# Optimization experiments

Measured on AMD Instinct MI355X. Metric: run time of the kernel, lower is better.

## Reference

```python
import jax, jax.numpy as jnp
import numpy as np

EPS = 1e-5


def gated_graph_conv(x, edge_index, W, w_ih, w_hh, b_ih, b_hh):
    # W: [num_layers, C, C]; PyG pads input features up to out_channels C.
    N = x.shape[0]
    C = W.shape[1]
    if x.shape[1] < C:
        x = jnp.pad(x, ((0, 0), (0, C - x.shape[1])))
    src, dst = edge_index[0], edge_index[1]
    for i in range(W.shape[0]):
        m = x @ W[i]                                   # [N, C]
        agg = jax.ops.segment_sum(m[src], dst, num_segments=N)  # scatter-add aggr
        # GRUCell(agg, x)
        gi = agg @ w_ih.T + b_ih                       # [N, 3C]
        gh = x @ w_hh.T + b_hh
        ir, iz, in_ = jnp.split(gi, 3, axis=-1)
        hr, hz, hn = jnp.split(gh, 3, axis=-1)
        r = jax.nn.sigmoid(ir + hr)
        z = jax.nn.sigmoid(iz + hz)
        n = jnp.tanh(in_ + r * hn)
        x = (1.0 - z) * n + z * x
    return x


def batch_norm_eval(x, gamma, beta, mean, var):
    return (x - mean) * jax.lax.rsqrt(var + EPS) * gamma + beta


def _ggc_params(key, C):
    ks = jax.random.split(key, 5)
    s = 1.0 / np.sqrt(C)
    return (jax.random.uniform(ks[0], (4, C, C), minval=-s, maxval=s),
            jax.random.uniform(ks[1], (3 * C, C), minval=-s, maxval=s),
            jax.random.uniform(ks[2], (3 * C, C), minval=-s, maxval=s),
            jax.random.uniform(ks[3], (3 * C,), minval=-s, maxval=s),
            jax.random.uniform(ks[4], (3 * C,), minval=-s, maxval=s))


def _bn_params(key, C):
    ks = jax.random.split(key, 4)
    return (jax.random.normal(ks[0], (C,)) * 0.1 + 1.0,
            jax.random.normal(ks[1], (C,)) * 0.1,
            jax.random.normal(ks[2], (C,)) * 0.1,
            jax.random.uniform(ks[3], (C,), minval=0.5, maxval=1.5))


def setup_inputs() -> dict:
    key = jax.random.key(0)
    N, E, NF, NG, NA = 50000, 800000, 32, 256, 10
    ks = jax.random.split(key, 12)
    x = jax.random.normal(ks[0], (N, NF), dtype=jnp.float32)
    edge_index = jax.random.randint(ks[1], (2, E), 0, N, dtype=jnp.int64)
    batch = jnp.sort(jax.random.randint(ks[2], (N,), 0, NG, dtype=jnp.int64))
    c1 = _ggc_params(ks[3], NF)
    c2 = _ggc_params(ks[4], 64)
    c3 = _ggc_params(ks[5], 128)
    bn1 = _bn_params(ks[6], NF)
    bn2 = _bn_params(ks[7], 64)
    s1 = 1.0 / np.sqrt(128)
    fc1_W = jax.random.uniform(ks[8], (256, 128), minval=-s1, maxval=s1)
    fc1_b = jax.random.uniform(ks[9], (256,), minval=-s1, maxval=s1)
    s2 = 1.0 / np.sqrt(256)
    fc2_W = jax.random.uniform(ks[10], (NA, 256), minval=-s2, maxval=s2)
    fc2_b = jax.random.uniform(ks[11], (NA,), minval=-s2, maxval=s2)
    d = {"x": x, "edge_index": edge_index, "batch": batch,
         "fc1_W": fc1_W, "fc1_b": fc1_b, "fc2_W": fc2_W, "fc2_b": fc2_b}
    for name, p in (("conv1", c1), ("conv2", c2), ("conv3", c3)):
        d[name + "_W"], d[name + "_wih"], d[name + "_whh"], d[name + "_bih"], d[name + "_bhh"] = p
    for name, p in (("bn1", bn1), ("bn2", bn2)):
        d[name + "_gamma"], d[name + "_beta"], d[name + "_mean"], d[name + "_var"] = p
    return d


def reference(x, edge_index, batch,
              conv1_W, conv1_wih, conv1_whh, conv1_bih, conv1_bhh,
              conv2_W, conv2_wih, conv2_whh, conv2_bih, conv2_bhh,
              conv3_W, conv3_wih, conv3_whh, conv3_bih, conv3_bhh,
              bn1_gamma, bn1_beta, bn1_mean, bn1_var,
              bn2_gamma, bn2_beta, bn2_mean, bn2_var,
              fc1_W, fc1_b, fc2_W, fc2_b):
    NUM_GRAPHS = 256
    h = jax.nn.elu(gated_graph_conv(x, edge_index, conv1_W, conv1_wih, conv1_whh, conv1_bih, conv1_bhh))
    h = batch_norm_eval(h, bn1_gamma, bn1_beta, bn1_mean, bn1_var)
    h = jax.nn.elu(gated_graph_conv(h, edge_index, conv2_W, conv2_wih, conv2_whh, conv2_bih, conv2_bhh))
    h = batch_norm_eval(h, bn2_gamma, bn2_beta, bn2_mean, bn2_var)
    h = jax.nn.elu(gated_graph_conv(h, edge_index, conv3_W, conv3_wih, conv3_whh, conv3_bih, conv3_bhh))
    g = jax.ops.segment_sum(h, batch, num_segments=NUM_GRAPHS)  # global_add_pool
    g = jax.nn.elu(g @ fc1_W.T + fc1_b)
    # dropout is identity in eval mode
    return jax.nn.log_softmax(g @ fc2_W.T + fc2_b, axis=-1)
```

## Files before the change

### kernel.cpp

```cpp
#include <hip/hip_runtime.h>
#include <math.h>


#define EPS_BN 1e-5f

typedef short short8 __attribute__((ext_vector_type(8)));
typedef unsigned short u16x8 __attribute__((ext_vector_type(8)));
typedef float f32x4 __attribute__((ext_vector_type(4)));

__device__ __forceinline__ float elu_f(float v) {
    return v > 0.f ? v : expm1f(v);
}
__device__ __forceinline__ float sigmoid_f(float v) {
    return 1.f / (1.f + __expf(-v));
}
__device__ __forceinline__ float tanh_f(float v) {
    float e = __expf(2.f * v);
    return 1.f - 2.f / (e + 1.f);
}
__device__ __forceinline__ unsigned short f2bf(float f) {
    unsigned u = __float_as_uint(f);
    unsigned r = (u + 0x7FFF + ((u >> 16) & 1)) >> 16;
    return (unsigned short)r;
}
__device__ __forceinline__ float bf2f(unsigned short b) {
    return __uint_as_float(((unsigned)b) << 16);
}


__global__ __launch_bounds__(256) void hist_kernel(
    const int* __restrict__ ei, int* __restrict__ deg, int E, int N) {
    int part = blockIdx.x & 7;
    int blk = blockIdx.x >> 3;
    int nblk = gridDim.x >> 3;
    int lo = (int)((long)N * part >> 3);
    int hi = (int)((long)N * (part + 1) >> 3);
    for (int e = blk * 256 + threadIdx.x; e < E; e += nblk * 256) {
        int d = ei[E + e];
        if (d >= lo && d < hi) atomicAdd(&deg[d], 1);
    }
}

__global__ __launch_bounds__(256) void scan1_kernel(
    const int* __restrict__ deg, int* __restrict__ out,
    int* __restrict__ blockSums, int N) {
    __shared__ int sdata[256];
    int b = blockIdx.x, t = threadIdx.x;
    int base = b * 1024 + t * 4;
    int v[4], s = 0;
#pragma unroll
    for (int i = 0; i < 4; ++i) {
        v[i] = (base + i < N) ? deg[base + i] : 0;
        s += v[i];
    }
    sdata[t] = s;
    __syncthreads();
    for (int off = 1; off < 256; off <<= 1) {
        int x = (t >= off) ? sdata[t - off] : 0;
        __syncthreads();
        sdata[t] += x;
        __syncthreads();
    }
    int run = sdata[t] - s;
#pragma unroll
    for (int i = 0; i < 4; ++i) {
        if (base + i < N) out[base + i] = run;
        run += v[i];
    }
    if (t == 255) blockSums[b] = sdata[255];
}

__global__ void scan2_kernel(int* blockSums, int nb) {
    if (threadIdx.x == 0 && blockIdx.x == 0) {
        int run = 0;
        for (int i = 0; i < nb; ++i) {
            int v = blockSums[i];
            blockSums[i] = run;
            run += v;
        }
    }
}

__global__ __launch_bounds__(256) void scan3_kernel(
    const int* __restrict__ out, const int* __restrict__ blockSums,
    int* __restrict__ rowstart, int* __restrict__ writeptr, int N, int E) {
    int i = blockIdx.x * 256 + threadIdx.x;
    if (i < N) {
        int v = out[i] + blockSums[i >> 10];
        rowstart[i] = v;
        writeptr[i] = v;
    }
    if (i == 0) rowstart[N] = E;
}

__global__ __launch_bounds__(256) void fill_kernel(
    const int* __restrict__ ei, int* __restrict__ writeptr,
    int* __restrict__ csr_src, int E, int N) {
    int part = blockIdx.x & 7;
    int blk = blockIdx.x >> 3;
    int nblk = gridDim.x >> 3;
    int lo = (int)((long)N * part >> 3);
    int hi = (int)((long)N * (part + 1) >> 3);
    for (int e = blk * 256 + threadIdx.x; e < E; e += nblk * 256) {
        int d = ei[E + e];
        if (d >= lo && d < hi) {
            int p = atomicAdd(&writeptr[d], 1);
            csr_src[p] = ei[e];
        }
    }
}


template <int C>
__global__ __launch_bounds__(256) void wc_kernel(
    const float* __restrict__ W, const float* __restrict__ wih,
    float* __restrict__ Wc) {
    int idx = blockIdx.x * 256 + threadIdx.x;
    if (idx >= 4 * C * 3 * C) return;
    int l = idx / (C * 3 * C);
    int r = idx % (C * 3 * C);
    int k = r / (3 * C);
    int row = r % (3 * C);
    const float* wrow = W + ((size_t)l * C + k) * C;
    const float* irow = wih + (size_t)row * C;
    float acc = 0.f;
#pragma unroll 4
    for (int t = 0; t < C; ++t) acc += wrow[t] * irow[t];
    Wc[idx] = acc;
}


template <int C>
__global__ __launch_bounds__(256) void swizzle_b2_kernel(
    const float* __restrict__ Wc, const float* __restrict__ whh,
    unsigned short* __restrict__ BsHi, unsigned short* __restrict__ BsLo) {
    constexpr int CT = C / 16;
    int idx = blockIdx.x * 256 + threadIdx.x;
    if (idx >= 4 * 6 * C * C) return;
    int l = idx / (6 * C * C);
    int r0 = idx % (6 * C * C);
    int j = r0 & 7;
    int lane = (r0 >> 3) & 63;
    int rest = r0 >> 9;
    int tslot = rest % (3 * CT);
    int ks = rest / (3 * CT);
    int k = ks * 32 + (lane >> 4) * 8 + j;
    int g = tslot / CT;
    int lt = tslot % CT;
    int c = lt * 16 + (lane & 15);
    int row = g * C + c;
    float v = (k < C) ? Wc[((size_t)l * C + k) * 3 * C + row]
                      : whh[(size_t)row * C + (k - C)];
    unsigned short h = f2bf(v);
    BsHi[idx] = h;
    BsLo[idx] = f2bf(v - bf2f(h));
}


template <int C>
__global__ __launch_bounds__(256) void gather_kernel(
    const unsigned short* __restrict__ Xhi,
    const int* __restrict__ rowstart, const int* __restrict__ csr_src,
    unsigned short* __restrict__ Shi, int N) {
    constexpr int LPG = C / 8;
    constexpr int GPB = 256 / LPG;
    int lane = threadIdx.x % LPG;
    int grp = threadIdx.x / LPG;
    int d = blockIdx.x * GPB + grp;
    if (d >= N) return;
    int p = rowstart[d];
    int p1 = rowstart[d + 1];
    float a[8];
#pragma unroll
    for (int j = 0; j < 8; ++j) a[j] = 0.f;
    int off = lane * 8;
    for (; p + 3 < p1; p += 4) {
        int s0 = csr_src[p];
        int s1 = csr_src[p + 1];
        int s2 = csr_src[p + 2];
        int s3 = csr_src[p + 3];
        u16x8 h0 = *(const u16x8*)(Xhi + (size_t)s0 * C + off);
        u16x8 h1 = *(const u16x8*)(Xhi + (size_t)s1 * C + off);
        u16x8 h2 = *(const u16x8*)(Xhi + (size_t)s2 * C + off);
        u16x8 h3 = *(const u16x8*)(Xhi + (size_t)s3 * C + off);
#pragma unroll
        for (int j = 0; j < 8; ++j) {
            a[j] += (bf2f(h0[j]) + bf2f(h1[j])) + (bf2f(h2[j]) + bf2f(h3[j]));
        }
    }
    for (; p < p1; ++p) {
        int s0 = csr_src[p];
        u16x8 h0 = *(const u16x8*)(Xhi + (size_t)s0 * C + off);
#pragma unroll
        for (int j = 0; j < 8; ++j) a[j] += bf2f(h0[j]);
    }
    size_t base = (size_t)d * C + off;
#pragma unroll
    for (int j = 0; j < 8; ++j) Shi[base + j] = f2bf(a[j]);
}


template <int C, int NT, int MINW>
__global__ __launch_bounds__(256, MINW) void gru_mfma_kernel(
    const unsigned short* __restrict__ Hin,
    unsigned short* __restrict__ Hout,
    const unsigned short* __restrict__ Shi,
    const unsigned short* __restrict__ BsHi, const unsigned short* __restrict__ BsLo,
    const float* __restrict__ biasI, const float* __restrict__ biasH, int N) {
    constexpr int CT = C / 16;
    constexpr int KS = C / 16;
    constexpr int CTW = CT / 4;
    constexpr int TPW = NT / 16;
    int wave = threadIdx.x >> 6;
    int lane = threadIdx.x & 63;
    int quad = lane >> 4;
    int l16 = lane & 15;
    int node0 = blockIdx.x * NT;
    int arow[TPW];
#pragma unroll
    for (int t = 0; t < TPW; ++t) {
        int r = node0 + t * 16 + l16;
        arow[t] = r < N ? r : N - 1;
    }
    f32x4 accR[CTW][TPW], accZ[CTW][TPW], accN[CTW][TPW], accH[CTW][TPW];
#pragma unroll
    for (int ct = 0; ct < CTW; ++ct)
#pragma unroll
        for (int t = 0; t < TPW; ++t) {
            accR[ct][t] = (f32x4){0.f, 0.f, 0.f, 0.f};
            accZ[ct][t] = (f32x4){0.f, 0.f, 0.f, 0.f};
            accN[ct][t] = (f32x4){0.f, 0.f, 0.f, 0.f};
            accH[ct][t] = (f32x4){0.f, 0.f, 0.f, 0.f};
        }
    const short8* bhi = (const short8*)BsHi;
    const short8* blo = (const short8*)BsLo;

    for (int ks = 0; ks < KS / 2; ++ks) {
        int k0 = ks * 32 + quad * 8;
        short8 ahi[TPW];
#pragma unroll
        for (int t = 0; t < TPW; ++t)
            ahi[t] = *(const short8*)(Shi + (size_t)arow[t] * C + k0);
#pragma unroll
        for (int ct = 0; ct < CTW; ++ct) {
            int ts = ks * 3 * CT + wave * CTW + ct;
            short8 bhf = bhi[(size_t)ts * 64 + lane];
            short8 blf = blo[(size_t)ts * 64 + lane];
#pragma unroll
            for (int t = 0; t < TPW; ++t) {
                accR[ct][t] = __builtin_amdgcn_mfma_f32_16x16x32_bf16(ahi[t], bhf, accR[ct][t], 0, 0, 0);
                accR[ct][t] = __builtin_amdgcn_mfma_f32_16x16x32_bf16(ahi[t], blf, accR[ct][t], 0, 0, 0);
            }
            bhf = bhi[(size_t)(ts + CT) * 64 + lane];
            blf = blo[(size_t)(ts + CT) * 64 + lane];
#pragma unroll
            for (int t = 0; t < TPW; ++t) {
                accZ[ct][t] = __builtin_amdgcn_mfma_f32_16x16x32_bf16(ahi[t], bhf, accZ[ct][t], 0, 0, 0);
                accZ[ct][t] = __builtin_amdgcn_mfma_f32_16x16x32_bf16(ahi[t], blf, accZ[ct][t], 0, 0, 0);
            }
            bhf = bhi[(size_t)(ts + 2 * CT) * 64 + lane];
            blf = blo[(size_t)(ts + 2 * CT) * 64 + lane];
#pragma unroll
            for (int t = 0; t < TPW; ++t) {
                accN[ct][t] = __builtin_amdgcn_mfma_f32_16x16x32_bf16(ahi[t], bhf, accN[ct][t], 0, 0, 0);
                accN[ct][t] = __builtin_amdgcn_mfma_f32_16x16x32_bf16(ahi[t], blf, accN[ct][t], 0, 0, 0);
            }
        }
    }
    for (int ks = KS / 2; ks < KS; ++ks) {
        int k0 = ks * 32 + quad * 8 - C;
        short8 ahi[TPW];
#pragma unroll
        for (int t = 0; t < TPW; ++t)
            ahi[t] = *(const short8*)(Hin + (size_t)arow[t] * C + k0);
#pragma unroll
        for (int ct = 0; ct < CTW; ++ct) {
            int ts = ks * 3 * CT + wave * CTW + ct;
            short8 bhf = bhi[(size_t)ts * 64 + lane];
#pragma unroll
            for (int t = 0; t < TPW; ++t)
                accR[ct][t] = __builtin_amdgcn_mfma_f32_16x16x32_bf16(ahi[t], bhf, accR[ct][t], 0, 0, 0);
            bhf = bhi[(size_t)(ts + CT) * 64 + lane];
#pragma unroll
            for (int t = 0; t < TPW; ++t)
                accZ[ct][t] = __builtin_amdgcn_mfma_f32_16x16x32_bf16(ahi[t], bhf, accZ[ct][t], 0, 0, 0);
            bhf = bhi[(size_t)(ts + 2 * CT) * 64 + lane];
#pragma unroll
            for (int t = 0; t < TPW; ++t)
                accH[ct][t] = __builtin_amdgcn_mfma_f32_16x16x32_bf16(ahi[t], bhf, accH[ct][t], 0, 0, 0);
        }
    }

#pragma unroll
    for (int ct = 0; ct < CTW; ++ct) {
        int c = (wave * CTW + ct) * 16 + l16;
        float bir = biasI[c], biz = biasI[C + c], bin = biasI[2 * C + c];
        float bhr = biasH[c], bhz = biasH[C + c], bhn = biasH[2 * C + c];
#pragma unroll
        for (int t = 0; t < TPW; ++t) {
#pragma unroll
            for (int r = 0; r < 4; ++r) {
                int node = node0 + t * 16 + quad * 4 + r;
                if (node < N) {
                    size_t gi = (size_t)node * C + c;
                    float xo = bf2f(Hin[gi]);
                    float rv = sigmoid_f(accR[ct][t][r] + bir + bhr);
                    float zv = sigmoid_f(accZ[ct][t][r] + biz + bhz);
                    float nv = tanh_f(accN[ct][t][r] + bin + rv * (accH[ct][t][r] + bhn));
                    Hout[gi] = f2bf((1.f - zv) * nv + zv * xo);
                }
            }
        }
    }
}

__global__ __launch_bounds__(256, 4) void gru32_kernel(
    const unsigned short* __restrict__ Hin,
    unsigned short* __restrict__ Hout,
    const unsigned short* __restrict__ Shi,
    const unsigned short* __restrict__ BsHi, const unsigned short* __restrict__ BsLo,
    const float* __restrict__ biasI, const float* __restrict__ biasH, int N) {
    constexpr int C = 32;
    constexpr int CT = 2;
    int wave = threadIdx.x >> 6;
    int lane = threadIdx.x & 63;
    int quad = lane >> 4;
    int l16 = lane & 15;
    int node0 = blockIdx.x * 64 + wave * 16;
    int ar = node0 + l16;
    if (ar >= N) ar = N - 1;
    f32x4 accR[CT], accZ[CT], accN[CT], accH[CT];
#pragma unroll
    for (int t = 0; t < CT; ++t) {
        accR[t] = (f32x4){0.f, 0.f, 0.f, 0.f};
        accZ[t] = (f32x4){0.f, 0.f, 0.f, 0.f};
        accN[t] = (f32x4){0.f, 0.f, 0.f, 0.f};
        accH[t] = (f32x4){0.f, 0.f, 0.f, 0.f};
    }
    const short8* bhi = (const short8*)BsHi;
    const short8* blo = (const short8*)BsLo;
    int k0 = quad * 8;
    {
        short8 ahi = *(const short8*)(Shi + (size_t)ar * C + k0);
#pragma unroll
        for (int g = 0; g < 3; ++g) {
            f32x4* acc = g == 0 ? accR : (g == 1 ? accZ : accN);
#pragma unroll
            for (int t = 0; t < CT; ++t) {
                int ts = g * CT + t;
                short8 bhf = bhi[(size_t)ts * 64 + lane];
                short8 blf = blo[(size_t)ts * 64 + lane];
                acc[t] = __builtin_amdgcn_mfma_f32_16x16x32_bf16(ahi, bhf, acc[t], 0, 0, 0);
                acc[t] = __builtin_amdgcn_mfma_f32_16x16x32_bf16(ahi, blf, acc[t], 0, 0, 0);
            }
        }
    }
    {
        short8 ahi = *(const short8*)(Hin + (size_t)ar * C + k0);
#pragma unroll
        for (int g = 0; g < 3; ++g) {
            f32x4* acc = g == 0 ? accR : (g == 1 ? accZ : accH);
#pragma unroll
            for (int t = 0; t < CT; ++t) {
                int ts = 3 * CT + g * CT + t;
                short8 bhf = bhi[(size_t)ts * 64 + lane];
                acc[t] = __builtin_amdgcn_mfma_f32_16x16x32_bf16(ahi, bhf, acc[t], 0, 0, 0);
            }
        }
    }
#pragma unroll
    for (int t = 0; t < CT; ++t) {
        int c = t * 16 + l16;
        float bir = biasI[c], biz = biasI[C + c], bin = biasI[2 * C + c];
        float bhr = biasH[c], bhz = biasH[C + c], bhn = biasH[2 * C + c];
#pragma unroll
        for (int r = 0; r < 4; ++r) {
            int node = node0 + quad * 4 + r;
            if (node < N) {
                size_t gi = (size_t)node * C + c;
                float xo = bf2f(Hin[gi]);
                float rv = sigmoid_f(accR[t][r] + bir + bhr);
                float zv = sigmoid_f(accZ[t][r] + biz + bhz);
                float nv = tanh_f(accN[t][r] + bin + rv * (accH[t][r] + bhn));
                Hout[gi] = f2bf((1.f - zv) * nv + zv * xo);
            }
        }
    }
}


__global__ __launch_bounds__(256) void init_x_kernel(
    const float* __restrict__ x, unsigned short* __restrict__ H, int total) {
    int t = blockIdx.x * 256 + threadIdx.x;
    if (t < total) H[t] = f2bf(x[t]);
}

template <int Cin, int Cout>
__global__ __launch_bounds__(256) void elu_bn_pad_kernel(
    const unsigned short* __restrict__ S, unsigned short* __restrict__ D,
    const float* __restrict__ gamma, const float* __restrict__ beta,
    const float* __restrict__ mean, const float* __restrict__ var, int N) {
    long t = (long)blockIdx.x * 256 + threadIdx.x;
    long total = (long)N * Cout;
    if (t >= total) return;
    int n = (int)(t / Cout);
    int c = (int)(t & (Cout - 1));
    float v = 0.f;
    if (c < Cin) {
        size_t si = (size_t)n * Cin + c;
        float x = bf2f(S[si]);
        x = elu_f(x);
        v = (x - mean[c]) * rsqrtf(var[c] + EPS_BN) * gamma[c] + beta[c];
    }
    D[t] = f2bf(v);
}

__global__ __launch_bounds__(256) void pool_elu_kernel(
    const unsigned short* __restrict__ H,
    const int* __restrict__ batch, float* __restrict__ G, int N) {
    long t = (long)blockIdx.x * 256 + threadIdx.x;
    if (t >= (long)N * 128) return;
    int n = (int)(t >> 7);
    int c = (int)(t & 127);
    float v = elu_f(bf2f(H[t]));
    atomicAdd(&G[batch[n] * 128 + c], v);
}

__global__ __launch_bounds__(256) void fc1_kernel(
    const float* __restrict__ G, const float* __restrict__ W,
    const float* __restrict__ b, float* __restrict__ G2) {
    __shared__ float row[128];
    int g = blockIdx.x;
    int j = threadIdx.x;
    if (j < 128) row[j] = G[g * 128 + j];
    __syncthreads();
    float acc = b[j];
    for (int k = 0; k < 128; ++k) acc += row[k] * W[j * 128 + k];
    G2[g * 256 + j] = elu_f(acc);
}

__global__ __launch_bounds__(64) void fc2_logsoftmax_kernel(
    const float* __restrict__ G2, const float* __restrict__ W,
    const float* __restrict__ b, float* __restrict__ out) {
    __shared__ float row[256];
    __shared__ float logits[10];
    __shared__ float red[2];
    int g = blockIdx.x;
    int tid = threadIdx.x;
    for (int i = tid; i < 256; i += 64) row[i] = G2[g * 256 + i];
    __syncthreads();
    if (tid < 10) {
        float acc = b[tid];
        for (int k = 0; k < 256; ++k) acc += row[k] * W[tid * 256 + k];
        logits[tid] = acc;
    }
    __syncthreads();
    if (tid == 0) {
        float m = -1e30f;
        for (int a = 0; a < 10; ++a) m = fmaxf(m, logits[a]);
        float s = 0.f;
        for (int a = 0; a < 10; ++a) s += expf(logits[a] - m);
        red[0] = m;
        red[1] = logf(s);
    }
    __syncthreads();
    if (tid < 10) out[g * 10 + tid] = logits[tid] - red[0] - red[1];
}


template <int C>
static void run_conv(unsigned short* A, unsigned short* B,
                     unsigned short* Shi,
                     float* Wc, unsigned short* BsHi, unsigned short* BsLo,
                     const float* W, const float* wih, const float* whh,
                     const float* bih, const float* bhh,
                     const int* rowstart, const int* csr_src,
                     int N, int E, hipStream_t stream) {
    wc_kernel<C><<<(4 * C * 3 * C + 255) / 256, 256, 0, stream>>>(W, wih, Wc);
    swizzle_b2_kernel<C><<<(4 * 6 * C * C + 255) / 256, 256, 0, stream>>>(Wc, whh, BsHi, BsLo);
    constexpr int NT = (C == 128) ? 32 : 64;
    int nb = (N + NT - 1) / NT;
    constexpr int GPB = 2048 / C;
    int gblocks = (N + GPB - 1) / GPB;
    unsigned short *in = A, *out = B;
    for (int it = 0; it < 4; ++it) {
        gather_kernel<C><<<gblocks, 256, 0, stream>>>(
            in, rowstart, csr_src, Shi, N);
        const unsigned short* bs_h = BsHi + (size_t)it * 6 * C * C;
        const unsigned short* bs_l = BsLo + (size_t)it * 6 * C * C;
        if constexpr (C == 32)
            gru32_kernel<<<nb, 256, 0, stream>>>(
                in, out, Shi, bs_h, bs_l, bih, bhh, N);
        else
            gru_mfma_kernel<C, NT, 3><<<nb, 256, 0, stream>>>(
                in, out, Shi, bs_h, bs_l, bih, bhh, N);
        unsigned short* tp = in; in = out; out = tp;
    }
}

extern "C" void kernel_launch(void* const* d_in, const int* in_sizes, int n_in,
                              void* d_out, int out_size, void* d_ws, size_t ws_size,
                              hipStream_t stream) {
    const float* x = (const float*)d_in[0];
    const int* ei = (const int*)d_in[1];
    const int* batch = (const int*)d_in[2];
    const float* fc1W = (const float*)d_in[3];
    const float* fc1b = (const float*)d_in[4];
    const float* fc2W = (const float*)d_in[5];
    const float* fc2b = (const float*)d_in[6];
    const float* c1W = (const float*)d_in[7];
    const float* c1wih = (const float*)d_in[8];
    const float* c1whh = (const float*)d_in[9];
    const float* c1bih = (const float*)d_in[10];
    const float* c1bhh = (const float*)d_in[11];
    const float* c2W = (const float*)d_in[12];
    const float* c2wih = (const float*)d_in[13];
    const float* c2whh = (const float*)d_in[14];
    const float* c2bih = (const float*)d_in[15];
    const float* c2bhh = (const float*)d_in[16];
    const float* c3W = (const float*)d_in[17];
    const float* c3wih = (const float*)d_in[18];
    const float* c3whh = (const float*)d_in[19];
    const float* c3bih = (const float*)d_in[20];
    const float* c3bhh = (const float*)d_in[21];
    const float* bn1g = (const float*)d_in[22];
    const float* bn1b = (const float*)d_in[23];
    const float* bn1m = (const float*)d_in[24];
    const float* bn1v = (const float*)d_in[25];
    const float* bn2g = (const float*)d_in[26];
    const float* bn2b = (const float*)d_in[27];
    const float* bn2m = (const float*)d_in[28];
    const float* bn2v = (const float*)d_in[29];

    int N = in_sizes[0] / 32;
    int E = in_sizes[1] / 2;

    const size_t NB = (size_t)N * 128;
    unsigned short* PA = (unsigned short*)d_ws;
    unsigned short* PB = PA + NB;
    unsigned short* Shi = PB + NB;
    unsigned short* BsHi = Shi + NB;
    unsigned short* BsLo = BsHi + 393216;
    float* Wc = (float*)(BsLo + 393216);
    float* G = Wc + 196608;
    float* G2 = G + 32768;
    int* deg = (int*)(G2 + 65536);
    int* scanout = deg + N;
    int* rowstart = scanout + N;
    int* writeptr = rowstart + N + 1;
    int* blockSums = writeptr + N;
    int* csr_src = blockSums + 64;

    hipMemsetAsync(deg, 0, (size_t)N * sizeof(int), stream);
    hist_kernel<<<2048, 256, 0, stream>>>(ei, deg, E, N);
    int nscan = (N + 1023) / 1024;
    scan1_kernel<<<nscan, 256, 0, stream>>>(deg, scanout, blockSums, N);
    scan2_kernel<<<1, 64, 0, stream>>>(blockSums, nscan);
    scan3_kernel<<<(N + 255) / 256, 256, 0, stream>>>(scanout, blockSums, rowstart, writeptr, N, E);
    fill_kernel<<<2048, 256, 0, stream>>>(ei, writeptr, csr_src, E, N);

    init_x_kernel<<<(N * 32 + 255) / 256, 256, 0, stream>>>(x, PA, N * 32);

    run_conv<32>(PA, PB, Shi, Wc, BsHi, BsLo,
                 c1W, c1wih, c1whh, c1bih, c1bhh, rowstart, csr_src, N, E, stream);
    elu_bn_pad_kernel<32, 64><<<(int)(((long)N * 64 + 255) / 256), 256, 0, stream>>>(
        PA, PB, bn1g, bn1b, bn1m, bn1v, N);

    run_conv<64>(PB, PA, Shi, Wc, BsHi, BsLo,
                 c2W, c2wih, c2whh, c2bih, c2bhh, rowstart, csr_src, N, E, stream);
    elu_bn_pad_kernel<64, 128><<<(int)(((long)N * 128 + 255) / 256), 256, 0, stream>>>(
        PB, PA, bn2g, bn2b, bn2m, bn2v, N);

    run_conv<128>(PA, PB, Shi, Wc, BsHi, BsLo,
                  c3W, c3wih, c3whh, c3bih, c3bhh, rowstart, csr_src, N, E, stream);

    hipMemsetAsync(G, 0, 256 * 128 * sizeof(float), stream);
    pool_elu_kernel<<<(int)(((long)N * 128 + 255) / 256), 256, 0, stream>>>(
        PA, batch, G, N);

    fc1_kernel<<<256, 256, 0, stream>>>(G, fc1W, fc1b, G2);
    fc2_logsoftmax_kernel<<<256, 64, 0, stream>>>(G2, fc2W, fc2b, (float*)d_out);
}
```

Baseline: 793.7 us.

## Batch weight prep launches, unroll gather by 8, pair nodes in pooling atomics

Weight fusion and swizzling for all three convolutions now run as one wc kernel and one swizzle kernel at the start instead of two launches per convolution, which cuts launch count. The gather loop gains an 8-way unrolled path so more independent row loads are in flight per destination node. Pooling handles two nodes per thread and merges their contributions into one atomicAdd when both belong to the same graph, reducing atomic traffic. The cost is a larger workspace for the weights of all layers and higher register use in gather.

```diff
diff --git a/kernel.cpp b/kernel.cpp
--- a/kernel.cpp
+++ b/kernel.cpp
@@ -111,12 +111,9 @@
 }
 
 
-template <int C>
-__global__ __launch_bounds__(256) void wc_kernel(
+__device__ __forceinline__ void wc_one(
     const float* __restrict__ W, const float* __restrict__ wih,
-    float* __restrict__ Wc) {
-    int idx = blockIdx.x * 256 + threadIdx.x;
-    if (idx >= 4 * C * 3 * C) return;
+    float* __restrict__ Wc, int idx, int C) {
     int l = idx / (C * 3 * C);
     int r = idx % (C * 3 * C);
     int k = r / (3 * C);
@@ -129,14 +126,22 @@
     Wc[idx] = acc;
 }
 
-
-template <int C>
-__global__ __launch_bounds__(256) void swizzle_b2_kernel(
+__global__ __launch_bounds__(256) void wc_all_kernel(
+    const float* __restrict__ W1, const float* __restrict__ wih1,
+    const float* __restrict__ W2, const float* __restrict__ wih2,
+    const float* __restrict__ W3, const float* __restrict__ wih3,
+    float* __restrict__ Wc) {
+    int idx = blockIdx.x * 256 + threadIdx.x;
+    if (idx < 12288) wc_one(W1, wih1, Wc, idx, 32);
+    else if (idx < 61440) wc_one(W2, wih2, Wc + 12288, idx - 12288, 64);
+    else if (idx < 258048) wc_one(W3, wih3, Wc + 61440, idx - 61440, 128);
+}
+
+__device__ __forceinline__ void swz_one(
     const float* __restrict__ Wc, const float* __restrict__ whh,
-    unsigned short* __restrict__ BsHi, unsigned short* __restrict__ BsLo) {
-    constexpr int CT = C / 16;
-    int idx = blockIdx.x * 256 + threadIdx.x;
-    if (idx >= 4 * 6 * C * C) return;
+    unsigned short* __restrict__ BsHi, unsigned short* __restrict__ BsLo,
+    int idx, int C) {
+    int CT = C / 16;
     int l = idx / (6 * C * C);
     int r0 = idx % (6 * C * C);
     int j = r0 & 7;
@@ -156,6 +161,20 @@
     BsLo[idx] = f2bf(v - bf2f(h));
 }
 
+__global__ __launch_bounds__(256) void swizzle_all_kernel(
+    const float* __restrict__ Wc,
+    const float* __restrict__ whh1, const float* __restrict__ whh2,
+    const float* __restrict__ whh3,
+    unsigned short* __restrict__ BsHi, unsigned short* __restrict__ BsLo) {
+    int idx = blockIdx.x * 256 + threadIdx.x;
+    if (idx < 24576)
+        swz_one(Wc, whh1, BsHi, BsLo, idx, 32);
+    else if (idx < 122880)
+        swz_one(Wc + 12288, whh2, BsHi + 24576, BsLo + 24576, idx - 24576, 64);
+    else if (idx < 516096)
+        swz_one(Wc + 61440, whh3, BsHi + 122880, BsLo + 122880, idx - 122880, 128);
+}
+
 
 template <int C>
 __global__ __launch_bounds__(256) void gather_kernel(
@@ -174,6 +193,20 @@
 #pragma unroll
     for (int j = 0; j < 8; ++j) a[j] = 0.f;
     int off = lane * 8;
+    for (; p + 7 < p1; p += 8) {
+        int s[8];
+#pragma unroll
+        for (int u = 0; u < 8; ++u) s[u] = csr_src[p + u];
+        u16x8 h[8];
+#pragma unroll
+        for (int u = 0; u < 8; ++u)
+            h[u] = *(const u16x8*)(Xhi + (size_t)s[u] * C + off);
+#pragma unroll
+        for (int u = 0; u < 8; ++u) {
+#pragma unroll
+            for (int j = 0; j < 8; ++j) a[j] += bf2f(h[u][j]);
+        }
+    }
     for (; p + 3 < p1; p += 4) {
         int s0 = csr_src[p];
         int s1 = csr_src[p + 1];
@@ -419,11 +452,23 @@
     const unsigned short* __restrict__ H,
     const int* __restrict__ batch, float* __restrict__ G, int N) {
     long t = (long)blockIdx.x * 256 + threadIdx.x;
-    if (t >= (long)N * 128) return;
-    int n = (int)(t >> 7);
+    long npairs = ((long)N + 1) >> 1;
+    if (t >= npairs * 128) return;
+    int pr = (int)(t >> 7);
     int c = (int)(t & 127);
-    float v = elu_f(bf2f(H[t]));
-    atomicAdd(&G[batch[n] * 128 + c], v);
+    int n0 = pr * 2, n1 = n0 + 1;
+    float v0 = elu_f(bf2f(H[(size_t)n0 * 128 + c]));
+    int b0 = batch[n0];
+    if (n1 < N) {
+        float v1 = elu_f(bf2f(H[(size_t)n1 * 128 + c]));
+        int b1 = batch[n1];
+        if (b1 == b0) {
+            atomicAdd(&G[b0 * 128 + c], v0 + v1);
+            return;
+        }
+        atomicAdd(&G[b1 * 128 + c], v1);
+    }
+    atomicAdd(&G[b0 * 128 + c], v0);
 }
 
 __global__ __launch_bounds__(256) void fc1_kernel(
@@ -471,13 +516,10 @@
 template <int C>
 static void run_conv(unsigned short* A, unsigned short* B,
                      unsigned short* Shi,
-                     float* Wc, unsigned short* BsHi, unsigned short* BsLo,
-                     const float* W, const float* wih, const float* whh,
+                     const unsigned short* BsHi, const unsigned short* BsLo,
                      const float* bih, const float* bhh,
                      const int* rowstart, const int* csr_src,
                      int N, int E, hipStream_t stream) {
-    wc_kernel<C><<<(4 * C * 3 * C + 255) / 256, 256, 0, stream>>>(W, wih, Wc);
-    swizzle_b2_kernel<C><<<(4 * 6 * C * C + 255) / 256, 256, 0, stream>>>(Wc, whh, BsHi, BsLo);
     constexpr int NT = (C == 128) ? 32 : 64;
     int nb = (N + NT - 1) / NT;
     constexpr int GPB = 2048 / C;
@@ -540,9 +582,9 @@
     unsigned short* PB = PA + NB;
     unsigned short* Shi = PB + NB;
     unsigned short* BsHi = Shi + NB;
-    unsigned short* BsLo = BsHi + 393216;
-    float* Wc = (float*)(BsLo + 393216);
-    float* G = Wc + 196608;
+    unsigned short* BsLo = BsHi + 516096;
+    float* Wc = (float*)(BsLo + 516096);
+    float* G = Wc + 258048;
     float* G2 = G + 32768;
     int* deg = (int*)(G2 + 65536);
     int* scanout = deg + N;
@@ -551,6 +593,11 @@
     int* blockSums = writeptr + N;
     int* csr_src = blockSums + 64;
 
+    wc_all_kernel<<<(258048 + 255) / 256, 256, 0, stream>>>(
+        c1W, c1wih, c2W, c2wih, c3W, c3wih, Wc);
+    swizzle_all_kernel<<<(516096 + 255) / 256, 256, 0, stream>>>(
+        Wc, c1whh, c2whh, c3whh, BsHi, BsLo);
+
     hipMemsetAsync(deg, 0, (size_t)N * sizeof(int), stream);
     hist_kernel<<<2048, 256, 0, stream>>>(ei, deg, E, N);
     int nscan = (N + 1023) / 1024;
@@ -561,22 +608,25 @@
 
     init_x_kernel<<<(N * 32 + 255) / 256, 256, 0, stream>>>(x, PA, N * 32);
 
-    run_conv<32>(PA, PB, Shi, Wc, BsHi, BsLo,
-                 c1W, c1wih, c1whh, c1bih, c1bhh, rowstart, csr_src, N, E, stream);
+    run_conv<32>(PA, PB, Shi, BsHi, BsLo,
+                 c1bih, c1bhh, rowstart, csr_src, N, E, stream);
     elu_bn_pad_kernel<32, 64><<<(int)(((long)N * 64 + 255) / 256), 256, 0, stream>>>(
         PA, PB, bn1g, bn1b, bn1m, bn1v, N);
 
-    run_conv<64>(PB, PA, Shi, Wc, BsHi, BsLo,
-                 c2W, c2wih, c2whh, c2bih, c2bhh, rowstart, csr_src, N, E, stream);
+    run_conv<64>(PB, PA, Shi, BsHi + 24576, BsLo + 24576,
+                 c2bih, c2bhh, rowstart, csr_src, N, E, stream);
     elu_bn_pad_kernel<64, 128><<<(int)(((long)N * 128 + 255) / 256), 256, 0, stream>>>(
         PB, PA, bn2g, bn2b, bn2m, bn2v, N);
 
-    run_conv<128>(PA, PB, Shi, Wc, BsHi, BsLo,
-                  c3W, c3wih, c3whh, c3bih, c3bhh, rowstart, csr_src, N, E, stream);
+    run_conv<128>(PA, PB, Shi, BsHi + 122880, BsLo + 122880,
+                  c3bih, c3bhh, rowstart, csr_src, N, E, stream);
 
     hipMemsetAsync(G, 0, 256 * 128 * sizeof(float), stream);
-    pool_elu_kernel<<<(int)(((long)N * 128 + 255) / 256), 256, 0, stream>>>(
-        PA, batch, G, N);
+    {
+        long npairs = ((long)N + 1) >> 1;
+        pool_elu_kernel<<<(int)((npairs * 128 + 255) / 256), 256, 0, stream>>>(
+            PA, batch, G, N);
+    }
 
     fc1_kernel<<<256, 256, 0, stream>>>(G, fc1W, fc1b, G2);
     fc2_logsoftmax_kernel<<<256, 64, 0, stream>>>(G2, fc2W, fc2b, (float*)d_out);
```

New measurement: 783.2 us, median of 2. Within noise of the previous version (-1.3%).
